# Kernel optimization log

Measured on AMD Instinct MI355X. Metric: run time of the kernel, lower is better.

Reference implementation:

```python
import jax, jax.numpy as jnp
import numpy as np

HEADS = 8
DIM_HEAD = 64
SCALE = DIM_HEAD ** -0.5


def setup_inputs() -> dict:
    key = jax.random.key(0)
    k1, k2, k3 = jax.random.split(key, 3)
    b, n, dim = 2, 4096, 512
    inner = HEADS * DIM_HEAD
    x = jax.random.normal(k1, (b, n, dim), dtype=jnp.float32)
    w_qkv = jax.random.normal(k2, (dim, 3 * inner), dtype=jnp.float32) * (dim ** -0.5)
    w_out = jax.random.normal(k3, (inner, dim), dtype=jnp.float32) * (inner ** -0.5)
    b_out = jnp.zeros((dim,), dtype=jnp.float32)
    return {"x": x, "w_qkv": w_qkv, "w_out": w_out, "b_out": b_out}


def reference(x, w_qkv, w_out, b_out):
    b, n, dim = x.shape
    qkv = x @ w_qkv  # [b, n, 3*inner]
    q, k, v = jnp.split(qkv, 3, axis=-1)
    # b n (h d) -> b h n d
    split_heads = lambda t: t.reshape(b, n, HEADS, DIM_HEAD).transpose(0, 2, 1, 3)
    q, k, v = split_heads(q), split_heads(k), split_heads(v)
    dots = jnp.einsum('bhid,bhjd->bhij', q, k) * SCALE  # [b, h, n, n]
    attn = jax.nn.log_softmax(dots, axis=-1)  # NOTE: log-softmax, not softmax
    out = jnp.einsum('bhij,bhjd->bhid', attn, v)  # [b, h, n, d]
    out = out.transpose(0, 2, 1, 3).reshape(b, n, HEADS * DIM_HEAD)
    return out @ w_out + b_out + x
```

## Files before the change

### kernel.cpp

```cpp
#include <hip/hip_runtime.h>
#include <stdint.h>

#define NSEQ   4096
#define BATCH  2
#define NHEAD  8
#define DHEAD  64
#define DIM    512
#define NQKV   1536
#define MROWS  (BATCH*NSEQ)
#define NBH    (BATCH*NHEAD)

typedef float  f32x4 __attribute__((ext_vector_type(4)));
typedef short  s16x8 __attribute__((ext_vector_type(8)));

__device__ __forceinline__ unsigned short f2b(float f){
  unsigned int u = __float_as_uint(f);
  u += 0x7FFFu + ((u >> 16) & 1u);
  return (unsigned short)(u >> 16);
}
__device__ __forceinline__ float b2f(unsigned short h){
  return __uint_as_float(((unsigned int)h) << 16);
}
__device__ __forceinline__ void gld_lds16(const void* g, void* l){
  __builtin_amdgcn_global_load_lds((const __attribute__((address_space(1))) unsigned int*)g,
                                   (__attribute__((address_space(3))) unsigned int*)l, 16, 0, 0);
}

__global__ void k_prep(const float* __restrict__ x, unsigned short* __restrict__ xb,
                       const float* __restrict__ wqkv, unsigned short* __restrict__ wqT,
                       const float* __restrict__ wout, unsigned short* __restrict__ woT){
  __shared__ float t[32][33];
  const int b = blockIdx.x;
  if (b < 4096){
    const int i = b*256 + threadIdx.x;
    float4 v = ((const float4*)x)[i];
    ushort4 o;
    o.x = f2b(v.x); o.y = f2b(v.y); o.z = f2b(v.z); o.w = f2b(v.w);
    ((ushort4*)xb)[i] = o;
  } else {
    const float* in; unsigned short* out; int R, C, cb, rb;
    if (b < 4096 + 768){
      const int q = b - 4096; in = wqkv; out = wqT; R = DIM; C = NQKV;
      cb = (q % 48)*32; rb = (q / 48)*32;
    } else {
      const int q = b - 4096 - 768; in = wout; out = woT; R = DIM; C = DIM;
      cb = (q & 15)*32; rb = (q >> 4)*32;
    }
    const int tx = threadIdx.x & 31, ty = threadIdx.x >> 5;
    #pragma unroll
    for (int s = 0; s < 32; s += 8) t[ty+s][tx] = in[(size_t)(rb+ty+s)*C + cb + tx];
    __syncthreads();
    #pragma unroll
    for (int s = 0; s < 32; s += 8) out[(size_t)(cb+ty+s)*R + rb + tx] = f2b(t[tx][ty+s]);
  }
}

#define QSTAGE(KS, B) do{ \
    const int k0_ = (KS)*32; \
    _Pragma("unroll") \
    for (int i_ = 0; i_ < 2; ++i_){ \
      const int slot_ = w*2 + i_; \
      const int r_ = slot_*16 + (lane>>2); \
      const int ch_ = (lane&3) ^ (r_&3); \
      gld_lds16(A  + (size_t)(m0+r_)*DIM + k0_ + ch_*8, (char*)at[B] + slot_*1024); \
      gld_lds16(Bt + (size_t)(n0+r_)*DIM + k0_ + ch_*8, (char*)bt[B] + slot_*1024); \
    }}while(0)

__global__ __launch_bounds__(256) void k_qkv_gemm(
    const unsigned short* __restrict__ A,
    const unsigned short* __restrict__ Bt,
    unsigned short* __restrict__ qbuf, unsigned short* __restrict__ kbuf,
    unsigned short* __restrict__ vbuf){
  __shared__ __align__(16) unsigned short at[2][128*32];
  __shared__ __align__(16) unsigned short bt[2][128*32];
  const int n0 = blockIdx.x*128, m0 = blockIdx.y*128;
  const int tid = threadIdx.x, w = tid>>6, lane = tid&63;
  const int wr = (w>>1)*64, wc = (w&1)*64;
  f32x4 acc[4][4] = {};
  QSTAGE(0, 0);
  for (int ks = 0; ks < 16; ++ks){
    __syncthreads();
    if (ks < 15) QSTAGE(ks+1, (ks+1)&1);
    const unsigned short* atc = at[ks&1];
    const unsigned short* btc = bt[ks&1];
    s16x8 af[4], bfr[4];
    #pragma unroll
    for (int f = 0; f < 4; ++f){
      const int rr = wr + f*16 + (lane&15);
      af[f]  = *(const s16x8*)((const char*)atc + rr*64 + ((((lane>>4)) ^ (rr&3))<<4));
      const int cc = wc + f*16 + (lane&15);
      bfr[f] = *(const s16x8*)((const char*)btc + cc*64 + ((((lane>>4)) ^ (cc&3))<<4));
    }
    #pragma unroll
    for (int fr = 0; fr < 4; ++fr)
      #pragma unroll
      for (int fc = 0; fc < 4; ++fc)
        acc[fr][fc] = __builtin_amdgcn_mfma_f32_16x16x32_bf16(bfr[fc], af[fr], acc[fr][fc], 0,0,0);
  }
  const float QS = 0.18033688011112042f;
  #pragma unroll
  for (int fr = 0; fr < 4; ++fr){
    const int row = m0 + wr + fr*16 + (lane&15);
    const int b = row >> 12, n = row & 4095;
    #pragma unroll
    for (int fc = 0; fc < 4; ++fc){
      const int col0 = n0 + wc + fc*16 + ((lane>>4)<<2);
      const int which = col0 >> 9;
      const int h = (col0 & 511) >> 6;
      const int d = col0 & 63;
      unsigned short* dst = (which==0) ? qbuf : ((which==1) ? kbuf : vbuf);
      const float sc = (which==0) ? QS : 1.f;
      ushort4 o;
      o.x = f2b(acc[fr][fc][0]*sc);
      o.y = f2b(acc[fr][fc][1]*sc);
      o.z = f2b(acc[fr][fc][2]*sc);
      o.w = f2b(acc[fr][fc][3]*sc);
      *(ushort4*)(dst + (size_t)((b*NHEAD + h)*NSEQ + n)*DHEAD + d) = o;
    }
  }
}

__global__ __launch_bounds__(256) void k_tpart(
    const unsigned short* __restrict__ kbuf, const unsigned short* __restrict__ vbuf,
    unsigned short* __restrict__ tpart, float* __restrict__ vsp){
  __shared__ __align__(16) unsigned short kt[64*64];
  __shared__ __align__(16) unsigned short vt[64*64];
  const int bh = blockIdx.y, jc = blockIdx.x;
  const unsigned short* K = kbuf + (size_t)bh*NSEQ*DHEAD;
  const unsigned short* V = vbuf + (size_t)bh*NSEQ*DHEAD;
  const int tid = threadIdx.x;
  const int d1 = (tid>>4)<<2, d2 = (tid&15)<<2;
  const int j0 = jc*64;
  #pragma unroll
  for (int c = 0; c < 2; ++c){
    const int q = tid + 256*c;
    const int row = q>>3, ch = q&7;
    *(float4*)((char*)kt + row*128 + ch*16) = *(const float4*)((const char*)K + (size_t)(j0+row)*128 + ch*16);
    *(float4*)((char*)vt + row*128 + ch*16) = *(const float4*)((const char*)V + (size_t)(j0+row)*128 + ch*16);
  }
  __syncthreads();
  float accT[4][4] = {{0.f}};
  float accV[4] = {0.f,0.f,0.f,0.f};
  for (int jj = 0; jj < 64; ++jj){
    const ushort4 k4 = *(const ushort4*)(kt + jj*64 + d1);
    const ushort4 v4 = *(const ushort4*)(vt + jj*64 + d2);
    float kf[4] = {b2f(k4.x), b2f(k4.y), b2f(k4.z), b2f(k4.w)};
    float vf[4] = {b2f(v4.x), b2f(v4.y), b2f(v4.z), b2f(v4.w)};
    #pragma unroll
    for (int a = 0; a < 4; ++a)
      #pragma unroll
      for (int b = 0; b < 4; ++b) accT[a][b] += kf[a]*vf[b];
    #pragma unroll
    for (int b = 0; b < 4; ++b) accV[b] += vf[b];
  }
  unsigned short* tp = tpart + ((size_t)bh*64 + jc)*4096;
  #pragma unroll
  for (int a = 0; a < 4; ++a)
    #pragma unroll
    for (int b = 0; b < 4; ++b) tp[(d1+a)*64 + (d2+b)] = f2b(accT[a][b]);
  if (tid < 16){
    #pragma unroll
    for (int b = 0; b < 4; ++b) vsp[((size_t)bh*64 + jc)*64 + d2 + b] = accV[b];
  }
}

__global__ void k_tred(const unsigned short* __restrict__ tpart, const float* __restrict__ vsp,
                       unsigned short* __restrict__ TB, float* __restrict__ vsum){
  const int blk = blockIdx.x;
  const int bh = blk >> 4, part = blk & 15;
  const int tid = threadIdx.x;
  const int idx = part*256 + tid;
  const int dd1 = idx>>6, dd2 = idx&63;
  float s = 0.f;
  #pragma unroll 8
  for (int pr = 0; pr < 64; ++pr) s += b2f(tpart[((size_t)bh*64 + pr)*4096 + idx]);
  TB[(size_t)bh*4096 + dd2*64 + dd1] = f2b(s);
  if (part == 0 && tid < 64){
    float v = 0.f;
    #pragma unroll 8
    for (int pr = 0; pr < 64; ++pr) v += vsp[((size_t)bh*64 + pr)*64 + tid];
    vsum[bh*64 + tid] = v;
  }
}

__global__ __launch_bounds__(256) void k_gmat(
    const unsigned short* __restrict__ TB, const float* __restrict__ vsum,
    const unsigned short* __restrict__ woT,
    unsigned short* __restrict__ Gt, float* __restrict__ vw){
  __shared__ __align__(16) unsigned short Tsh[64*64];
  __shared__ __align__(16) unsigned short wsh[64*64];
  const int bid = blockIdx.x;
  const int b = bid >> 6, h = (bid >> 3) & 7, ct = bid & 7;
  const int bh = b*8 + h, c0 = ct*64;
  const int tid = threadIdx.x;
  {
    const unsigned short* src = TB + (size_t)bh*4096;
    *(s16x8*)&Tsh[tid*16]     = *(const s16x8*)&src[tid*16];
    *(s16x8*)&Tsh[tid*16 + 8] = *(const s16x8*)&src[tid*16 + 8];
  }
  {
    const int c = tid & 63, d2b = (tid >> 6) << 4;
    const unsigned short* wr = woT + (size_t)(c0+c)*DIM + h*64 + d2b;
    s16x8 w0 = *(const s16x8*)wr;
    s16x8 w1 = *(const s16x8*)(wr+8);
    #pragma unroll
    for (int i = 0; i < 8; ++i){
      wsh[(d2b+i)*64 + c]   = w0[i];
      wsh[(d2b+8+i)*64 + c] = w1[i];
    }
  }
  __syncthreads();
  const int d1 = (tid>>4)<<2, cc = (tid&15)<<2;
  float accG[4][4] = {{0.f}};
  for (int d2 = 0; d2 < 64; ++d2){
    const ushort4 tv = *(const ushort4*)&Tsh[d2*64 + d1];
    const ushort4 wv = *(const ushort4*)&wsh[d2*64 + cc];
    float tf[4] = {b2f(tv.x), b2f(tv.y), b2f(tv.z), b2f(tv.w)};
    float wf[4] = {b2f(wv.x), b2f(wv.y), b2f(wv.z), b2f(wv.w)};
    #pragma unroll
    for (int a = 0; a < 4; ++a)
      #pragma unroll
      for (int bb = 0; bb < 4; ++bb) accG[a][bb] += tf[a]*wf[bb];
  }
  const float LN2 = 0.6931471805599453f;
  unsigned short* G = Gt + ((size_t)b*DIM + c0)*DIM + h*64;
  #pragma unroll
  for (int bb = 0; bb < 4; ++bb)
    #pragma unroll
    for (int a = 0; a < 4; ++a)
      G[(size_t)(cc+bb)*DIM + d1 + a] = f2b(accG[a][bb]*LN2);
  if (tid < 64){
    float s = 0.f;
    for (int d2 = 0; d2 < 64; ++d2) s += vsum[bh*64 + d2]*b2f(wsh[d2*64 + tid]);
    vw[(size_t)bh*DIM + c0 + tid] = s*LN2;
  }
}

#define ASTAGE(U, BUFI) do { \
    const int ti_ = jbase + (((U)+phase)&15); \
    const size_t o_ = (size_t)ti_*64*DHEAD; \
    char* d_ = (char*)kt[BUFI]; \
    gld_lds16(kg0 + o_, d_ + s0*1024); \
    gld_lds16(kg1 + o_, d_ + s1*1024); } while(0)

#define ATILE(BUFI) do { \
    const char* buf_ = (const char*)kt[BUFI]; \
    _Pragma("unroll") \
    for (int kk = 0; kk < 4; ++kk){ \
      const int r_ = kk*16 + (lane&15); \
      const s16x8 b0_ = *(const s16x8*)(buf_ + r_*128 + ((((lane>>4))   ^ (r_&7))<<4)); \
      const s16x8 b1_ = *(const s16x8*)(buf_ + r_*128 + (((4+(lane>>4)) ^ (r_&7))<<4)); \
      f32x4 a0_ = {0.f,0.f,0.f,0.f}, a1_ = {0.f,0.f,0.f,0.f}; \
      f32x4 a2_ = {0.f,0.f,0.f,0.f}, a3_ = {0.f,0.f,0.f,0.f}; \
      __builtin_amdgcn_s_setprio(1); \
      a0_ = __builtin_amdgcn_mfma_f32_16x16x32_bf16(aq[0][0], b0_, a0_, 0,0,0); \
      a0_ = __builtin_amdgcn_mfma_f32_16x16x32_bf16(aq[0][1], b1_, a0_, 0,0,0); \
      a1_ = __builtin_amdgcn_mfma_f32_16x16x32_bf16(aq[1][0], b0_, a1_, 0,0,0); \
      a1_ = __builtin_amdgcn_mfma_f32_16x16x32_bf16(aq[1][1], b1_, a1_, 0,0,0); \
      a2_ = __builtin_amdgcn_mfma_f32_16x16x32_bf16(aq[2][0], b0_, a2_, 0,0,0); \
      a2_ = __builtin_amdgcn_mfma_f32_16x16x32_bf16(aq[2][1], b1_, a2_, 0,0,0); \
      a3_ = __builtin_amdgcn_mfma_f32_16x16x32_bf16(aq[3][0], b0_, a3_, 0,0,0); \
      a3_ = __builtin_amdgcn_mfma_f32_16x16x32_bf16(aq[3][1], b1_, a3_, 0,0,0); \
      __builtin_amdgcn_s_setprio(0); \
      _Pragma("unroll") \
      for (int rr = 0; rr < 4; ++rr){ \
        lsum[0][rr] += __builtin_amdgcn_exp2f(a0_[rr]); \
        lsum[1][rr] += __builtin_amdgcn_exp2f(a1_[rr]); \
        lsum[2][rr] += __builtin_amdgcn_exp2f(a2_[rr]); \
        lsum[3][rr] += __builtin_amdgcn_exp2f(a3_[rr]); \
      } \
    } } while(0)

#define APHASE(U) do { \
    if ((U) <= 13)      { asm volatile("s_waitcnt vmcnt(4)" ::: "memory"); } \
    else if ((U) == 14) { asm volatile("s_waitcnt vmcnt(2)" ::: "memory"); } \
    else                { asm volatile("s_waitcnt vmcnt(0)" ::: "memory"); } \
    __builtin_amdgcn_s_barrier(); \
    asm volatile("" ::: "memory"); \
    if ((U) <= 12) ASTAGE((U)+3, ((U)+3)&3); \
    ATILE((U)&3); } while(0)

__global__ __launch_bounds__(256) void k_attn(
    const unsigned short* __restrict__ qbuf, const unsigned short* __restrict__ kbuf,
    float* __restrict__ ps){
  __shared__ __align__(16) unsigned short kt[4][64*64];
  const int bid = blockIdx.x;
  const int idx = bid >> 3;
  const int bh  = ((bid & 7) << 1) + (idx >> 6);
  const int rest = idx & 63;
  const int qchunk = rest >> 2;
  const int js = rest & 3;
  const int tid = threadIdx.x, w = tid>>6, lane = tid&63;
  const int q0 = qchunk*256 + w*64;
  const unsigned short* Q = qbuf + (size_t)bh*NSEQ*DHEAD;
  const unsigned short* K = kbuf + (size_t)bh*NSEQ*DHEAD;

  s16x8 aq[4][2];
  #pragma unroll
  for (int g = 0; g < 4; ++g){
    const int qrow = q0 + g*16 + (lane&15);
    aq[g][0] = *(const s16x8*)(Q + (size_t)qrow*DHEAD + ((lane>>4)<<3));
    aq[g][1] = *(const s16x8*)(Q + (size_t)qrow*DHEAD + 32 + ((lane>>4)<<3));
  }

  const int s0 = w*2, s1 = w*2 + 1;
  const int srow0 = s0*8 + (lane>>3), srow1 = s1*8 + (lane>>3);
  const int sch = ((lane&7) ^ (lane>>3));
  const unsigned short* kg0 = K + (size_t)srow0*DHEAD + sch*8;
  const unsigned short* kg1 = K + (size_t)srow1*DHEAD + sch*8;

  const int phase = (idx*5) & 15;
  const int jbase = js*16;

  ASTAGE(0, 0);
  ASTAGE(1, 1);
  ASTAGE(2, 2);

  float lsum[4][4] = {};
  APHASE(0);  APHASE(1);  APHASE(2);  APHASE(3);
  APHASE(4);  APHASE(5);  APHASE(6);  APHASE(7);
  APHASE(8);  APHASE(9);  APHASE(10); APHASE(11);
  APHASE(12); APHASE(13); APHASE(14); APHASE(15);

  #pragma unroll
  for (int m = 1; m < 16; m <<= 1)
    #pragma unroll
    for (int g = 0; g < 4; ++g)
      #pragma unroll
      for (int r = 0; r < 4; ++r) lsum[g][r] += __shfl_xor(lsum[g][r], m, 16);

  if ((lane&15) == 0){
    float* pp = ps + ((size_t)js*NBH + bh)*NSEQ;
    #pragma unroll
    for (int g = 0; g < 4; ++g)
      #pragma unroll
      for (int r = 0; r < 4; ++r)
        pp[q0 + g*16 + (lane>>4)*4 + r] = lsum[g][r];
  }
}

#define FSTAGE(KS, B) do{ \
    const int k0_ = (KS)*32; const int h_ = k0_>>6; const int kk_ = k0_&63; \
    _Pragma("unroll") \
    for (int i_ = 0; i_ < 2; ++i_){ \
      const int slot_ = w*2 + i_; \
      const int r_ = slot_*16 + (lane>>2); \
      const int ch_ = (lane&3) ^ (r_&3); \
      gld_lds16(Aq + ((size_t)h_*NSEQ + mrow0 + r_)*DHEAD + kk_ + ch_*8, (char*)at[B] + slot_*1024); \
      gld_lds16(Gb + (size_t)(n0+r_)*DIM + k0_ + ch_*8, (char*)bt[B] + slot_*1024); \
    }}while(0)

__global__ __launch_bounds__(256) void k_out_gemm(
    const unsigned short* __restrict__ qbuf,
    const unsigned short* __restrict__ Gt,
    const float* __restrict__ vw,
    const float* __restrict__ ps,
    const float* __restrict__ bias, const float* __restrict__ xres,
    float* __restrict__ out){
  __shared__ __align__(16) unsigned short at[2][128*32];
  __shared__ __align__(16) unsigned short bt[2][128*32];
  __shared__ float Lsh[128][9];
  __shared__ float vwsh[8][128];
  const int n0 = blockIdx.x*128, m0 = blockIdx.y*128;
  const int b = m0 >> 12, mrow0 = m0 & 4095;
  const int tid = threadIdx.x, w = tid>>6, lane = tid&63;
  const int wr = (w>>1)*64, wc = (w&1)*64;
  const unsigned short* Aq = qbuf + (size_t)b*NHEAD*NSEQ*DHEAD;
  const unsigned short* Gb = Gt + (size_t)b*DIM*DIM;

  f32x4 acc[4][4] = {};
  FSTAGE(0, 0);

  {
    const int rl = tid >> 1, h0 = (tid & 1) << 2;
    #pragma unroll
    for (int i = 0; i < 4; ++i){
      const int h = h0 + i;
      const float* pp = ps + (size_t)(b*NHEAD + h)*NSEQ + mrow0 + rl;
      const float s = (pp[0] + pp[(size_t)NBH*NSEQ]) +
                      (pp[(size_t)2*NBH*NSEQ] + pp[(size_t)3*NBH*NSEQ]);
      Lsh[rl][h] = log2f(s);
    }
    const int hh = tid >> 5, cl = (tid & 31) << 2;
    *(float4*)&vwsh[hh][cl] = *(const float4*)&vw[(size_t)(b*NHEAD + hh)*DIM + n0 + cl];
  }

  for (int ks = 0; ks < 16; ++ks){
    __syncthreads();
    if (ks < 15) FSTAGE(ks+1, (ks+1)&1);
    const unsigned short* atc = at[ks&1];
    const unsigned short* btc = bt[ks&1];
    s16x8 af[4], bfr[4];
    #pragma unroll
    for (int f = 0; f < 4; ++f){
      const int rr = wr + f*16 + (lane&15);
      af[f]  = *(const s16x8*)((const char*)atc + rr*64 + ((((lane>>4)) ^ (rr&3))<<4));
      const int cc = wc + f*16 + (lane&15);
      bfr[f] = *(const s16x8*)((const char*)btc + cc*64 + ((((lane>>4)) ^ (cc&3))<<4));
    }
    #pragma unroll
    for (int fr = 0; fr < 4; ++fr)
      #pragma unroll
      for (int fc = 0; fc < 4; ++fc)
        acc[fr][fc] = __builtin_amdgcn_mfma_f32_16x16x32_bf16(bfr[fc], af[fr], acc[fr][fc], 0,0,0);
  }

  float Lv[4][8];
  #pragma unroll
  for (int fr = 0; fr < 4; ++fr){
    const int rl = wr + fr*16 + (lane&15);
    #pragma unroll
    for (int h = 0; h < 8; ++h) Lv[fr][h] = Lsh[rl][h];
  }
  #pragma unroll
  for (int fr = 0; fr < 4; ++fr){
    const int row = m0 + wr + fr*16 + (lane&15);
    #pragma unroll
    for (int fc = 0; fc < 4; ++fc){
      const int cl0 = wc + fc*16 + ((lane>>4)<<2);
      const int col0 = n0 + cl0;
      float4 corr = {0.f,0.f,0.f,0.f};
      #pragma unroll
      for (int h = 0; h < 8; ++h){
        const float4 vv = *(const float4*)&vwsh[h][cl0];
        const float lh = Lv[fr][h];
        corr.x += lh*vv.x; corr.y += lh*vv.y; corr.z += lh*vv.z; corr.w += lh*vv.w;
      }
      const float4 bb = *(const float4*)&bias[col0];
      const float4 xr = *(const float4*)&xres[(size_t)row*DIM + col0];
      float4 o;
      o.x = acc[fr][fc][0] - corr.x + bb.x + xr.x;
      o.y = acc[fr][fc][1] - corr.y + bb.y + xr.y;
      o.z = acc[fr][fc][2] - corr.z + bb.z + xr.z;
      o.w = acc[fr][fc][3] - corr.w + bb.w + xr.w;
      *(float4*)&out[(size_t)row*DIM + col0] = o;
    }
  }
}

extern "C" void kernel_launch(void* const* d_in, const int* in_sizes, int n_in,
                              void* d_out, int out_size, void* d_ws, size_t ws_size,
                              hipStream_t stream){
  const float* x    = (const float*)d_in[0];
  const float* wqkv = (const float*)d_in[1];
  const float* wout = (const float*)d_in[2];
  const float* bout = (const float*)d_in[3];
  float* out = (float*)d_out;

  char* p = (char*)d_ws;
  unsigned short* xb   = (unsigned short*)p; p += (size_t)MROWS*DIM*2;
  unsigned short* wqT  = (unsigned short*)p; p += (size_t)NQKV*DIM*2;
  unsigned short* woT  = (unsigned short*)p; p += (size_t)DIM*DIM*2;
  unsigned short* qbuf = (unsigned short*)p; p += (size_t)NBH*NSEQ*DHEAD*2;
  unsigned short* kbuf = (unsigned short*)p; p += (size_t)NBH*NSEQ*DHEAD*2;
  unsigned short* vbuf = (unsigned short*)p; p += (size_t)NBH*NSEQ*DHEAD*2;
  unsigned short* tpart= (unsigned short*)p; p += (size_t)NBH*64*4096*2;
  float* vsp           = (float*)p;          p += (size_t)NBH*64*64*4;
  unsigned short* TB   = (unsigned short*)p; p += (size_t)NBH*64*64*2;
  float* vsum          = (float*)p;          p += (size_t)NBH*64*4;
  unsigned short* Gt   = (unsigned short*)p; p += (size_t)2*DIM*DIM*2;
  float* vw            = (float*)p;          p += (size_t)NBH*DIM*4;
  float* ps            = (float*)p;          p += (size_t)4*NBH*NSEQ*4;

  k_prep<<<dim3(4096 + 768 + 256), dim3(256), 0, stream>>>(x, xb, wqkv, wqT, wout, woT);
  k_qkv_gemm<<<dim3(NQKV/128, MROWS/128), dim3(256), 0, stream>>>(xb, wqT, qbuf, kbuf, vbuf);
  k_tpart<<<dim3(64, NBH), dim3(256), 0, stream>>>(kbuf, vbuf, tpart, vsp);
  k_tred<<<dim3(256), dim3(256), 0, stream>>>(tpart, vsp, TB, vsum);
  k_gmat<<<dim3(128), dim3(256), 0, stream>>>(TB, vsum, woT, Gt, vw);
  k_attn<<<dim3(1024), dim3(256), 0, stream>>>(qbuf, kbuf, ps);
  k_out_gemm<<<dim3(DIM/128, MROWS/128), dim3(256), 0, stream>>>(qbuf, Gt, vw, ps, bout, x, out);
}
```

Before: 130.1 us.

## Load K fragments directly from global into registers, dropping LDS staging

The attention-normalizer kernel stops staging K tiles through shared memory with async global-to-LDS loads and barriers. Each wave now reads its own K fragments straight from global memory into registers through a 4-deep software pipeline of register slots. This removes the LDS traffic and block-wide barriers, but every wave now fetches all K rows itself instead of sharing them across the block's 4 waves. The per-block phase rotation that staggered tile order is also dropped, so the fetches have less cache locality and higher L2 load.

```diff
diff --git a/kernel.cpp b/kernel.cpp
--- a/kernel.cpp
+++ b/kernel.cpp
@@ -236,54 +236,35 @@
   }
 }
 
-#define ASTAGE(U, BUFI) do { \
-    const int ti_ = jbase + (((U)+phase)&15); \
-    const size_t o_ = (size_t)ti_*64*DHEAD; \
-    char* d_ = (char*)kt[BUFI]; \
-    gld_lds16(kg0 + o_, d_ + s0*1024); \
-    gld_lds16(kg1 + o_, d_ + s1*1024); } while(0)
-
-#define ATILE(BUFI) do { \
-    const char* buf_ = (const char*)kt[BUFI]; \
+#define ALOAD(SL, T) do{ \
+    const unsigned short* p_ = kp + (size_t)(T)*1024; \
+    b0_##SL = *(const s16x8*)p_; \
+    b1_##SL = *(const s16x8*)(p_ + 32); }while(0)
+
+#define ACOMP(SL) do { \
+    f32x4 a0_ = {0.f,0.f,0.f,0.f}, a1_ = {0.f,0.f,0.f,0.f}; \
+    f32x4 a2_ = {0.f,0.f,0.f,0.f}, a3_ = {0.f,0.f,0.f,0.f}; \
+    __builtin_amdgcn_s_setprio(1); \
+    a0_ = __builtin_amdgcn_mfma_f32_16x16x32_bf16(aq[0][0], b0_##SL, a0_, 0,0,0); \
+    a0_ = __builtin_amdgcn_mfma_f32_16x16x32_bf16(aq[0][1], b1_##SL, a0_, 0,0,0); \
+    a1_ = __builtin_amdgcn_mfma_f32_16x16x32_bf16(aq[1][0], b0_##SL, a1_, 0,0,0); \
+    a1_ = __builtin_amdgcn_mfma_f32_16x16x32_bf16(aq[1][1], b1_##SL, a1_, 0,0,0); \
+    a2_ = __builtin_amdgcn_mfma_f32_16x16x32_bf16(aq[2][0], b0_##SL, a2_, 0,0,0); \
+    a2_ = __builtin_amdgcn_mfma_f32_16x16x32_bf16(aq[2][1], b1_##SL, a2_, 0,0,0); \
+    a3_ = __builtin_amdgcn_mfma_f32_16x16x32_bf16(aq[3][0], b0_##SL, a3_, 0,0,0); \
+    a3_ = __builtin_amdgcn_mfma_f32_16x16x32_bf16(aq[3][1], b1_##SL, a3_, 0,0,0); \
+    __builtin_amdgcn_s_setprio(0); \
     _Pragma("unroll") \
-    for (int kk = 0; kk < 4; ++kk){ \
-      const int r_ = kk*16 + (lane&15); \
-      const s16x8 b0_ = *(const s16x8*)(buf_ + r_*128 + ((((lane>>4))   ^ (r_&7))<<4)); \
-      const s16x8 b1_ = *(const s16x8*)(buf_ + r_*128 + (((4+(lane>>4)) ^ (r_&7))<<4)); \
-      f32x4 a0_ = {0.f,0.f,0.f,0.f}, a1_ = {0.f,0.f,0.f,0.f}; \
-      f32x4 a2_ = {0.f,0.f,0.f,0.f}, a3_ = {0.f,0.f,0.f,0.f}; \
-      __builtin_amdgcn_s_setprio(1); \
-      a0_ = __builtin_amdgcn_mfma_f32_16x16x32_bf16(aq[0][0], b0_, a0_, 0,0,0); \
-      a0_ = __builtin_amdgcn_mfma_f32_16x16x32_bf16(aq[0][1], b1_, a0_, 0,0,0); \
-      a1_ = __builtin_amdgcn_mfma_f32_16x16x32_bf16(aq[1][0], b0_, a1_, 0,0,0); \
-      a1_ = __builtin_amdgcn_mfma_f32_16x16x32_bf16(aq[1][1], b1_, a1_, 0,0,0); \
-      a2_ = __builtin_amdgcn_mfma_f32_16x16x32_bf16(aq[2][0], b0_, a2_, 0,0,0); \
-      a2_ = __builtin_amdgcn_mfma_f32_16x16x32_bf16(aq[2][1], b1_, a2_, 0,0,0); \
-      a3_ = __builtin_amdgcn_mfma_f32_16x16x32_bf16(aq[3][0], b0_, a3_, 0,0,0); \
-      a3_ = __builtin_amdgcn_mfma_f32_16x16x32_bf16(aq[3][1], b1_, a3_, 0,0,0); \
-      __builtin_amdgcn_s_setprio(0); \
-      _Pragma("unroll") \
-      for (int rr = 0; rr < 4; ++rr){ \
-        lsum[0][rr] += __builtin_amdgcn_exp2f(a0_[rr]); \
-        lsum[1][rr] += __builtin_amdgcn_exp2f(a1_[rr]); \
-        lsum[2][rr] += __builtin_amdgcn_exp2f(a2_[rr]); \
-        lsum[3][rr] += __builtin_amdgcn_exp2f(a3_[rr]); \
-      } \
+    for (int rr = 0; rr < 4; ++rr){ \
+      lsum[0][rr] += __builtin_amdgcn_exp2f(a0_[rr]); \
+      lsum[1][rr] += __builtin_amdgcn_exp2f(a1_[rr]); \
+      lsum[2][rr] += __builtin_amdgcn_exp2f(a2_[rr]); \
+      lsum[3][rr] += __builtin_amdgcn_exp2f(a3_[rr]); \
     } } while(0)
-
-#define APHASE(U) do { \
-    if ((U) <= 13)      { asm volatile("s_waitcnt vmcnt(4)" ::: "memory"); } \
-    else if ((U) == 14) { asm volatile("s_waitcnt vmcnt(2)" ::: "memory"); } \
-    else                { asm volatile("s_waitcnt vmcnt(0)" ::: "memory"); } \
-    __builtin_amdgcn_s_barrier(); \
-    asm volatile("" ::: "memory"); \
-    if ((U) <= 12) ASTAGE((U)+3, ((U)+3)&3); \
-    ATILE((U)&3); } while(0)
 
 __global__ __launch_bounds__(256) void k_attn(
     const unsigned short* __restrict__ qbuf, const unsigned short* __restrict__ kbuf,
     float* __restrict__ ps){
-  __shared__ __align__(16) unsigned short kt[4][64*64];
   const int bid = blockIdx.x;
   const int idx = bid >> 3;
   const int bh  = ((bid & 7) << 1) + (idx >> 6);
@@ -303,24 +284,19 @@
     aq[g][1] = *(const s16x8*)(Q + (size_t)qrow*DHEAD + 32 + ((lane>>4)<<3));
   }
 
-  const int s0 = w*2, s1 = w*2 + 1;
-  const int srow0 = s0*8 + (lane>>3), srow1 = s1*8 + (lane>>3);
-  const int sch = ((lane&7) ^ (lane>>3));
-  const unsigned short* kg0 = K + (size_t)srow0*DHEAD + sch*8;
-  const unsigned short* kg1 = K + (size_t)srow1*DHEAD + sch*8;
-
-  const int phase = (idx*5) & 15;
-  const int jbase = js*16;
-
-  ASTAGE(0, 0);
-  ASTAGE(1, 1);
-  ASTAGE(2, 2);
+  const unsigned short* kp = K + (size_t)(js*1024 + (lane&15))*DHEAD + ((lane>>4)<<3);
+
+  s16x8 b0_0, b1_0, b0_1, b1_1, b0_2, b1_2, b0_3, b1_3;
+  ALOAD(0, 0); ALOAD(1, 1); ALOAD(2, 2); ALOAD(3, 3);
 
   float lsum[4][4] = {};
-  APHASE(0);  APHASE(1);  APHASE(2);  APHASE(3);
-  APHASE(4);  APHASE(5);  APHASE(6);  APHASE(7);
-  APHASE(8);  APHASE(9);  APHASE(10); APHASE(11);
-  APHASE(12); APHASE(13); APHASE(14); APHASE(15);
+  for (int t = 0; t < 60; t += 4){
+    ACOMP(0); ALOAD(0, t+4);
+    ACOMP(1); ALOAD(1, t+5);
+    ACOMP(2); ALOAD(2, t+6);
+    ACOMP(3); ALOAD(3, t+7);
+  }
+  ACOMP(0); ACOMP(1); ACOMP(2); ACOMP(3);
 
   #pragma unroll
   for (int m = 1; m < 16; m <<= 1)
```

Result: slower. 147.0 us (+13.0%).
